# Optimization experiments

Measured on AMD Instinct MI355X. Metric: run time of the kernel, lower is better.

## Reference

```python
import jax, jax.numpy as jnp
import numpy as np

S, C1, C2, N = 4096, 2048, 2048, 1024


def setup_inputs() -> dict:
    key = jax.random.key(0)
    k1, k2, k3, k4 = jax.random.split(key, 4)
    # child log-likelihoods (samples, child_nodes); modest scale so exp() stays finite,
    # matching the (numerically naive) torch forward which exps without max-subtraction.
    ll1 = jax.random.normal(k1, (S, C1), dtype=jnp.float32)
    ll2 = jax.random.normal(k2, (S, C2), dtype=jnp.float32)
    # log edge weights, one tensor per child layer: (nodes, child_nodes)
    w1 = jax.random.normal(k3, (N, C1), dtype=jnp.float32)
    w2 = jax.random.normal(k4, (N, C2), dtype=jnp.float32)
    return {"ll1": ll1, "ll2": ll2, "w1": w1, "w2": w2}


def reference(ll1, ll2, w1, w2):
    # Per child layer: sum_c exp(ll[s,c] + w[n,c]) == exp(ll) @ exp(w).T  -> (S, N)
    # (same math as unsqueeze/repeat/exp/sum in the torch code, without the (S,C,N) blowup)
    result = jnp.exp(ll1) @ jnp.exp(w1).T + jnp.exp(ll2) @ jnp.exp(w2).T  # (S, N)
    # per-node log normalization constant over concatenated weights
    log_z = jax.nn.logsumexp(jnp.concatenate([w1, w2], axis=1), axis=1)  # (N,)
    return jnp.log(result) - log_z[None, :]
```

## Files before the change

kernel.cpp:

```cpp
#include <hip/hip_runtime.h>

#define S_DIM 4096
#define C_DIM 2048
#define N_DIM 1024
#define K_DIM 4096

#define BM2 256
#define BN2 256
#define KS 4
#define KSL (K_DIM / KS)
#define BK 32
#define NT2 (KSL / BK)
#define TILE2 32768
#define NBUF2 4

#define BM1 128
#define BN1 128
#define NT1 (K_DIM / BK)
#define TILE1 16384
#define NBUF1 8

typedef __attribute__((ext_vector_type(8))) short bf16x8;
typedef __attribute__((ext_vector_type(8))) unsigned short u16x8;
typedef __attribute__((ext_vector_type(4))) float f32x4;

__device__ static inline unsigned short f2bf(float f) {
    unsigned int u = __float_as_uint(f);
    u += 0x7FFFu + ((u >> 16) & 1u);
    return (unsigned short)(u >> 16);
}
__device__ static inline float bf2f(unsigned short h) {
    return __uint_as_float((unsigned int)h << 16);
}

__global__ void exp_ll_kernel(const float* __restrict__ ll1,
                              const float* __restrict__ ll2,
                              unsigned short* __restrict__ A) {
    const int total4 = S_DIM * C_DIM / 4;
    int stride = gridDim.x * blockDim.x;
    for (int i = blockIdx.x * blockDim.x + threadIdx.x; i < total4; i += stride) {
        int e = i << 2;
        int r = e >> 11;
        int c = e & 2047;
        size_t dst = ((size_t)r << 12) + c;
        float4 v = *reinterpret_cast<const float4*>(ll1 + e);
        ushort4 o;
        o.x = f2bf(__expf(v.x)); o.y = f2bf(__expf(v.y));
        o.z = f2bf(__expf(v.z)); o.w = f2bf(__expf(v.w));
        *reinterpret_cast<ushort4*>(A + dst) = o;
        float4 u = *reinterpret_cast<const float4*>(ll2 + e);
        ushort4 p;
        p.x = f2bf(__expf(u.x)); p.y = f2bf(__expf(u.y));
        p.z = f2bf(__expf(u.z)); p.w = f2bf(__expf(u.w));
        *reinterpret_cast<ushort4*>(A + dst + C_DIM) = p;
    }
}

__global__ void w_kernel(const float* __restrict__ w1,
                         const float* __restrict__ w2,
                         unsigned short* __restrict__ B,
                         float* __restrict__ lz) {
    const int n = blockIdx.x;
    const int tid = threadIdx.x;
    const int lane = tid & 63, wv = tid >> 6;
    const float* r1 = w1 + ((size_t)n << 11);
    const float* r2 = w2 + ((size_t)n << 11);
    float4 v0 = *reinterpret_cast<const float4*>(r1 + tid * 8);
    float4 v1 = *reinterpret_cast<const float4*>(r1 + tid * 8 + 4);
    float4 u0 = *reinterpret_cast<const float4*>(r2 + tid * 8);
    float4 u1 = *reinterpret_cast<const float4*>(r2 + tid * 8 + 4);

    float mx = fmaxf(fmaxf(fmaxf(v0.x, v0.y), fmaxf(v0.z, v0.w)),
                     fmaxf(fmaxf(v1.x, v1.y), fmaxf(v1.z, v1.w)));
    mx = fmaxf(mx, fmaxf(fmaxf(fmaxf(u0.x, u0.y), fmaxf(u0.z, u0.w)),
                          fmaxf(fmaxf(u1.x, u1.y), fmaxf(u1.z, u1.w))));
    #pragma unroll
    for (int off = 32; off > 0; off >>= 1) mx = fmaxf(mx, __shfl_xor(mx, off));
    __shared__ float red[4];
    if (lane == 0) red[wv] = mx;
    __syncthreads();
    mx = fmaxf(fmaxf(red[0], red[1]), fmaxf(red[2], red[3]));

    float s = __expf(v0.x - mx) + __expf(v0.y - mx) + __expf(v0.z - mx) + __expf(v0.w - mx)
            + __expf(v1.x - mx) + __expf(v1.y - mx) + __expf(v1.z - mx) + __expf(v1.w - mx)
            + __expf(u0.x - mx) + __expf(u0.y - mx) + __expf(u0.z - mx) + __expf(u0.w - mx)
            + __expf(u1.x - mx) + __expf(u1.y - mx) + __expf(u1.z - mx) + __expf(u1.w - mx);
    #pragma unroll
    for (int off = 32; off > 0; off >>= 1) s += __shfl_xor(s, off);
    __shared__ float red2[4];
    if (lane == 0) red2[wv] = s;
    __syncthreads();
    if (tid == 0)
        lz[n] = mx + __logf(red2[0] + red2[1] + red2[2] + red2[3]);

    unsigned short* brow = B + ((size_t)n << 12);
    ushort4 o;
    o.x = f2bf(__expf(v0.x)); o.y = f2bf(__expf(v0.y));
    o.z = f2bf(__expf(v0.z)); o.w = f2bf(__expf(v0.w));
    *reinterpret_cast<ushort4*>(brow + tid * 8) = o;
    o.x = f2bf(__expf(v1.x)); o.y = f2bf(__expf(v1.y));
    o.z = f2bf(__expf(v1.z)); o.w = f2bf(__expf(v1.w));
    *reinterpret_cast<ushort4*>(brow + tid * 8 + 4) = o;
    o.x = f2bf(__expf(u0.x)); o.y = f2bf(__expf(u0.y));
    o.z = f2bf(__expf(u0.z)); o.w = f2bf(__expf(u0.w));
    *reinterpret_cast<ushort4*>(brow + C_DIM + tid * 8) = o;
    o.x = f2bf(__expf(u1.x)); o.y = f2bf(__expf(u1.y));
    o.z = f2bf(__expf(u1.z)); o.w = f2bf(__expf(u1.w));
    *reinterpret_cast<ushort4*>(brow + C_DIM + tid * 8 + 4) = o;
}

typedef const unsigned int __attribute__((address_space(1)))* gas_ptr;
typedef unsigned int __attribute__((address_space(3)))* las_ptr;

__global__ __launch_bounds__(512, 1) void gemm_split_kernel(
        const unsigned short* __restrict__ A,
        const unsigned short* __restrict__ B,
        unsigned short* __restrict__ P) {
    __shared__ __align__(16) char lds[NBUF2 * TILE2];
    const int tid  = threadIdx.x;
    const int l    = tid & 63;
    const int w    = tid >> 6;
    const int wg   = blockIdx.x;
    const int x7   = wg & 7;
    const int bm   = (wg >> 3) & 15;
    const int c    = x7 + ((wg >> 7) << 3);
    const int ks   = c >> 2;
    const int bn   = c & 3;
    const int wr = w >> 1, wc = w & 1;
    const int lcol = l & 15, lk = l >> 4;

    const int kg = (l & 3) ^ ((l >> 3) & 3);
    const unsigned short* srcA0 = A + (size_t)(bm * BM2 + w * 16 + (l >> 2)) * K_DIM
                                    + ks * KSL + kg * 8;
    const unsigned short* srcA1 = srcA0 + (size_t)128 * K_DIM;
    const unsigned short* srcB0 = B + (size_t)(bn * BN2 + w * 16 + (l >> 2)) * K_DIM
                                    + ks * KSL + kg * 8;
    const unsigned short* srcB1 = srcB0 + (size_t)128 * K_DIM;
    const int dst0 = (w * 16 + (l >> 2)) * 64 + (l & 3) * 16;

    const int swz = (lk ^ ((lcol >> 1) & 3)) << 4;
    const int abase = (wr * 64 + lcol) * 64 + swz;
    const int bbase = 16384 + (wc * 128 + lcol) * 64 + swz;

    f32x4 acc[4][8] = {};
    bf16x8 a0[4], b0[8], a1[4], b1[8];

#define GLOAD(p_, o_) __builtin_amdgcn_global_load_lds((gas_ptr)(const void*)(p_), \
        (las_ptr)(void*)(lds + (o_)), 16, 0, 0)
#define STAGE2(T, BUFI) { const int _ko = (T) * BK; const int _bo = (BUFI) * TILE2;  \
        GLOAD(srcA0 + _ko, _bo + dst0);         GLOAD(srcA1 + _ko, _bo + dst0 + 8192); \
        GLOAD(srcB0 + _ko, _bo + dst0 + 16384); GLOAD(srcB1 + _ko, _bo + dst0 + 24576); }
#define READF2(RBUF, AR, BR) { const char* _rb = lds + (RBUF) * TILE2;               \
        _Pragma("unroll") for (int m = 0; m < 4; ++m)                                \
            AR[m] = *reinterpret_cast<const bf16x8*>(_rb + abase + m * 1024);        \
        _Pragma("unroll") for (int n = 0; n < 8; ++n)                                \
            BR[n] = *reinterpret_cast<const bf16x8*>(_rb + bbase + n * 1024); }
#define MFMAS2(AMM, BMM) {                                                           \
        __builtin_amdgcn_s_setprio(1);                                               \
        _Pragma("unroll") for (int m = 0; m < 4; ++m)                                \
            _Pragma("unroll") for (int n = 0; n < 8; ++n)                            \
                acc[m][n] = __builtin_amdgcn_mfma_f32_16x16x32_bf16(AMM[m], BMM[n],  \
                                                                    acc[m][n], 0, 0, 0); \
        __builtin_amdgcn_s_setprio(0); }
#define BODY2(RBUF, TS, SBUF, WAITN, DOSTAGE, AR, BR, AMM, BMM) {                    \
        asm volatile("s_waitcnt vmcnt(" #WAITN ")" ::: "memory");                    \
        __builtin_amdgcn_s_barrier();                                                \
        if (DOSTAGE) STAGE2(TS, SBUF);                                               \
        READF2(RBUF, AR, BR);                                                        \
        __builtin_amdgcn_sched_barrier(0);                                           \
        MFMAS2(AMM, BMM); }

    STAGE2(0, 0); STAGE2(1, 1); STAGE2(2, 2);
    asm volatile("s_waitcnt vmcnt(8)" ::: "memory");
    __builtin_amdgcn_s_barrier();
    READF2(0, a0, b0);
    for (int t4 = 0; t4 < NT2 - 4; t4 += 4) {
        BODY2(1, t4 + 3, 3, 4, 1, a1, b1, a0, b0);
        BODY2(2, t4 + 4, 0, 4, 1, a0, b0, a1, b1);
        BODY2(3, t4 + 5, 1, 4, 1, a1, b1, a0, b0);
        BODY2(0, t4 + 6, 2, 4, 1, a0, b0, a1, b1);
    }
    BODY2(1, 31, 3, 4, 1, a1, b1, a0, b0);
    BODY2(2, 0, 0, 4, 0, a0, b0, a1, b1);
    BODY2(3, 0, 0, 0, 0, a1, b1, a0, b0);
    MFMAS2(a1, b1);
#undef BODY2
#undef MFMAS2
#undef READF2
#undef STAGE2

    unsigned short* Pk = P + (size_t)ks * ((size_t)S_DIM * N_DIM);
    const int col_base = bn * BN2 + wc * 128;
    #pragma unroll
    for (int m = 0; m < 4; ++m) {
        const int row0 = bm * BM2 + wr * 64 + m * 16 + lk * 4;
        #pragma unroll
        for (int n = 0; n < 8; ++n) {
            const int col = col_base + n * 16 + lcol;
            #pragma unroll
            for (int j = 0; j < 4; ++j)
                Pk[(size_t)(row0 + j) * N_DIM + col] = f2bf(acc[m][n][j]);
        }
    }
#undef GLOAD
}

__global__ void reduce_kernel(const unsigned short* __restrict__ P,
                              const float* __restrict__ lz,
                              float* __restrict__ out) {
    const size_t SN = (size_t)S_DIM * N_DIM;
    int i = blockIdx.x * blockDim.x + threadIdx.x;
    size_t e = (size_t)i * 8;
    int n = (int)(e & (N_DIM - 1));
    u16x8 p0 = *reinterpret_cast<const u16x8*>(P + e);
    u16x8 p1 = *reinterpret_cast<const u16x8*>(P + SN + e);
    u16x8 p2 = *reinterpret_cast<const u16x8*>(P + 2 * SN + e);
    u16x8 p3 = *reinterpret_cast<const u16x8*>(P + 3 * SN + e);
    float4 lz0 = *reinterpret_cast<const float4*>(lz + n);
    float4 lz1 = *reinterpret_cast<const float4*>(lz + n + 4);
    float lzv[8] = {lz0.x, lz0.y, lz0.z, lz0.w, lz1.x, lz1.y, lz1.z, lz1.w};
    float o[8];
    #pragma unroll
    for (int j = 0; j < 8; ++j) {
        float s = bf2f((unsigned short)p0[j]) + bf2f((unsigned short)p1[j])
                + bf2f((unsigned short)p2[j]) + bf2f((unsigned short)p3[j]);
        o[j] = __logf(s) - lzv[j];
    }
    *reinterpret_cast<float4*>(out + e)     = make_float4(o[0], o[1], o[2], o[3]);
    *reinterpret_cast<float4*>(out + e + 4) = make_float4(o[4], o[5], o[6], o[7]);
}

__global__ __launch_bounds__(256, 1) void gemm_log_kernel128(
        const unsigned short* __restrict__ A,
        const unsigned short* __restrict__ B,
        const float* __restrict__ lz,
        float* __restrict__ out) {
    __shared__ __align__(16) char lds[NBUF1 * TILE1];
    const int tid  = threadIdx.x;
    const int l    = tid & 63;
    const int w    = tid >> 6;
    const int bn = blockIdx.x & 7;
    const int bm = blockIdx.x >> 3;
    const int wr = w >> 1, wc = w & 1;
    const int lcol = l & 15, lk = l >> 4;

    const int kg = (l & 3) ^ ((l >> 3) & 3);
    const unsigned short* src[4];
    int dst[4];
    #pragma unroll
    for (int i = 0; i < 4; ++i) {
        const int ri  = w * 4 + i;
        const int row = ri * 16 + (l >> 2);
        src[i] = (ri < 8)
            ? A + (size_t)(bm * BM1 + row) * K_DIM + kg * 8
            : B + (size_t)(bn * BN1 + row - 128) * K_DIM + kg * 8;
        dst[i] = row * 64 + (l & 3) * 16;
    }
    const int swz = (lk ^ ((lcol >> 1) & 3)) << 4;
    int aoff[4], boff[4];
    #pragma unroll
    for (int m = 0; m < 4; ++m) aoff[m] = (wr * 64 + m * 16 + lcol) * 64 + swz;
    #pragma unroll
    for (int n = 0; n < 4; ++n) boff[n] = 8192 + (wc * 64 + n * 16 + lcol) * 64 + swz;

    f32x4 acc[4][4] = {};
    bf16x8 a0[4], b0[4], a1[4], b1[4];

#define GLOAD(p_, o_) __builtin_amdgcn_global_load_lds((gas_ptr)(const void*)(p_), \
        (las_ptr)(void*)(lds + (o_)), 16, 0, 0)
#define STAGE(T, BUFI) { const int _ko = (T) * BK; const int _bo = (BUFI) * TILE1; \
        GLOAD(src[0] + _ko, _bo + dst[0]); GLOAD(src[1] + _ko, _bo + dst[1]);      \
        GLOAD(src[2] + _ko, _bo + dst[2]); GLOAD(src[3] + _ko, _bo + dst[3]); }
#define READF(RBUF, AR, BR) { const char* _rb = lds + (RBUF) * TILE1;              \
        _Pragma("unroll") for (int m = 0; m < 4; ++m)                              \
            AR[m] = *reinterpret_cast<const bf16x8*>(_rb + aoff[m]);               \
        _Pragma("unroll") for (int n = 0; n < 4; ++n)                              \
            BR[n] = *reinterpret_cast<const bf16x8*>(_rb + boff[n]); }
#define MFMAS(AMM, BMM)                                                            \
        _Pragma("unroll") for (int m = 0; m < 4; ++m)                              \
            _Pragma("unroll") for (int n = 0; n < 4; ++n)                          \
                acc[m][n] = __builtin_amdgcn_mfma_f32_16x16x32_bf16(AMM[m], BMM[n],\
                                                                    acc[m][n], 0, 0, 0);
#define BODY(T, SB, RB, WAITN, DOSTAGE, AR, BR, AMM, BMM) {                        \
        asm volatile("s_waitcnt vmcnt(" #WAITN ")" ::: "memory");                  \
        __builtin_amdgcn_s_barrier();                                              \
        if (DOSTAGE) STAGE((T) + 8, SB);                                           \
        READF(RB, AR, BR);                                                         \
        MFMAS(AMM, BMM); }

    STAGE(0, 0); STAGE(1, 1); STAGE(2, 2); STAGE(3, 3);
    STAGE(4, 4); STAGE(5, 5); STAGE(6, 6); STAGE(7, 7);
    asm volatile("s_waitcnt vmcnt(28)" ::: "memory");
    __builtin_amdgcn_s_barrier();
    READF(0, a0, b0);
    for (int t8 = 0; t8 < NT1 - 8; t8 += 8) {
        BODY(t8 + 0, 0, 1, 24, 1, a1, b1, a0, b0);
        BODY(t8 + 1, 1, 2, 24, 1, a0, b0, a1, b1);
        BODY(t8 + 2, 2, 3, 24, 1, a1, b1, a0, b0);
        BODY(t8 + 3, 3, 4, 24, 1, a0, b0, a1, b1);
        BODY(t8 + 4, 4, 5, 24, 1, a1, b1, a0, b0);
        BODY(t8 + 5, 5, 6, 24, 1, a0, b0, a1, b1);
        BODY(t8 + 6, 6, 7, 24, 1, a1, b1, a0, b0);
        BODY(t8 + 7, 7, 0, 24, 1, a0, b0, a1, b1);
    }
    BODY(120, 0, 1, 24, 0, a1, b1, a0, b0);
    BODY(121, 1, 2, 20, 0, a0, b0, a1, b1);
    BODY(122, 2, 3, 16, 0, a1, b1, a0, b0);
    BODY(123, 3, 4, 12, 0, a0, b0, a1, b1);
    BODY(124, 4, 5,  8, 0, a1, b1, a0, b0);
    BODY(125, 5, 6,  4, 0, a0, b0, a1, b1);
    BODY(126, 6, 7,  0, 0, a1, b1, a0, b0);
    MFMAS(a1, b1);
#undef BODY
#undef MFMAS
#undef READF
#undef STAGE
#undef GLOAD

    const int col_base = bn * BN1 + wc * 64;
    float lzv[4];
    #pragma unroll
    for (int n = 0; n < 4; ++n) lzv[n] = lz[col_base + n * 16 + lcol];
    #pragma unroll
    for (int m = 0; m < 4; ++m) {
        const int row0 = bm * BM1 + wr * 64 + m * 16 + lk * 4;
        #pragma unroll
        for (int n = 0; n < 4; ++n) {
            const int col = col_base + n * 16 + lcol;
            #pragma unroll
            for (int j = 0; j < 4; ++j)
                out[(size_t)(row0 + j) * N_DIM + col] = __logf(acc[m][n][j]) - lzv[n];
        }
    }
}

__global__ void naive_kernel(const float* __restrict__ ll1, const float* __restrict__ ll2,
                             const float* __restrict__ w1, const float* __restrict__ w2,
                             float* __restrict__ out) {
    int idx = blockIdx.x * blockDim.x + threadIdx.x;
    if (idx >= S_DIM * N_DIM) return;
    int s = idx >> 10, n = idx & (N_DIM - 1);
    const float* a1 = ll1 + (size_t)s * C_DIM;
    const float* a2 = ll2 + (size_t)s * C_DIM;
    const float* b1 = w1 + (size_t)n * C_DIM;
    const float* b2 = w2 + (size_t)n * C_DIM;
    float mx = -3.0e38f;
    for (int c = 0; c < C_DIM; ++c) mx = fmaxf(mx, b1[c]);
    for (int c = 0; c < C_DIM; ++c) mx = fmaxf(mx, b2[c]);
    float zs = 0.f, acc = 0.f;
    for (int c = 0; c < C_DIM; ++c) { zs += __expf(b1[c] - mx); acc += __expf(a1[c] + b1[c]); }
    for (int c = 0; c < C_DIM; ++c) { zs += __expf(b2[c] - mx); acc += __expf(a2[c] + b2[c]); }
    out[idx] = __logf(acc) - (mx + __logf(zs));
}

extern "C" void kernel_launch(void* const* d_in, const int* in_sizes, int n_in,
                              void* d_out, int out_size, void* d_ws, size_t ws_size,
                              hipStream_t stream) {
    const float* ll1 = (const float*)d_in[0];
    const float* ll2 = (const float*)d_in[1];
    const float* w1  = (const float*)d_in[2];
    const float* w2  = (const float*)d_in[3];
    float* out = (float*)d_out;

    const size_t a_elems = (size_t)S_DIM * K_DIM;
    const size_t b_elems = (size_t)N_DIM * K_DIM;
    const size_t sn      = (size_t)S_DIM * N_DIM;
    const size_t need1 = (a_elems + b_elems) * sizeof(unsigned short) + N_DIM * sizeof(float);
    const size_t need2 = need1 + KS * sn * sizeof(unsigned short);
    if (ws_size < need1) {
        naive_kernel<<<(S_DIM * N_DIM + 255) / 256, 256, 0, stream>>>(ll1, ll2, w1, w2, out);
        return;
    }
    unsigned short* Aws = (unsigned short*)d_ws;
    unsigned short* Bws = Aws + a_elems;
    float* lzws = (float*)(Bws + b_elems);

    exp_ll_kernel<<<2048, 256, 0, stream>>>(ll1, ll2, Aws);
    w_kernel<<<N_DIM, 256, 0, stream>>>(w1, w2, Bws, lzws);

    if (ws_size >= need2) {
        unsigned short* Pws = (unsigned short*)(lzws + N_DIM);
        gemm_split_kernel<<<(S_DIM / BM2) * (N_DIM / BN2) * KS, 512, 0, stream>>>(Aws, Bws, Pws);
        reduce_kernel<<<(int)(sn / 8 / 256), 256, 0, stream>>>(Pws, lzws, out);
    } else {
        gemm_log_kernel128<<<(S_DIM / BM1) * (N_DIM / BN1), 256, 0, stream>>>(Aws, Bws, lzws, out);
    }
}
```

Baseline: 78.91 us.

## Deepen GEMM LDS pipeline to five buffers and drop register double-buffering

The split-K GEMM kernel now keeps four tiles in flight using five LDS buffers instead of four, waiting on vmcnt(12) rather than vmcnt(4). The register ping-pong of A/B fragments, where the next tile's LDS reads overlapped the current tile's MFMAs under a sched_barrier, is replaced by a single fragment set read and consumed in the same step. The loop also uses runtime rotating buffer offsets instead of the manually unrolled four-way body. This hides more global load latency and frees registers, but exposes LDS read latency before the MFMAs, raises LDS use to 160KB which may limit occupancy, and adds per-iteration offset arithmetic.

```diff
diff --git a/kernel.cpp b/kernel.cpp
--- a/kernel.cpp
+++ b/kernel.cpp
@@ -12,7 +12,7 @@
 #define BK 32
 #define NT2 (KSL / BK)
 #define TILE2 32768
-#define NBUF2 4
+#define NBUF2 5
 
 #define BM1 128
 #define BN1 128
@@ -143,47 +143,44 @@
     const int bbase = 16384 + (wc * 128 + lcol) * 64 + swz;
 
     f32x4 acc[4][8] = {};
-    bf16x8 a0[4], b0[8], a1[4], b1[8];
+    bf16x8 a[4], b[8];
 
 #define GLOAD(p_, o_) __builtin_amdgcn_global_load_lds((gas_ptr)(const void*)(p_), \
         (las_ptr)(void*)(lds + (o_)), 16, 0, 0)
-#define STAGE2(T, BUFI) { const int _ko = (T) * BK; const int _bo = (BUFI) * TILE2;  \
+#define STAGE2(T, BO) { const int _ko = (T) * BK; const int _bo = (BO);              \
         GLOAD(srcA0 + _ko, _bo + dst0);         GLOAD(srcA1 + _ko, _bo + dst0 + 8192); \
         GLOAD(srcB0 + _ko, _bo + dst0 + 16384); GLOAD(srcB1 + _ko, _bo + dst0 + 24576); }
-#define READF2(RBUF, AR, BR) { const char* _rb = lds + (RBUF) * TILE2;               \
+#define READF2(BO) { const char* _rb = lds + (BO);                                   \
         _Pragma("unroll") for (int m = 0; m < 4; ++m)                                \
-            AR[m] = *reinterpret_cast<const bf16x8*>(_rb + abase + m * 1024);        \
+            a[m] = *reinterpret_cast<const bf16x8*>(_rb + abase + m * 1024);         \
         _Pragma("unroll") for (int n = 0; n < 8; ++n)                                \
-            BR[n] = *reinterpret_cast<const bf16x8*>(_rb + bbase + n * 1024); }
-#define MFMAS2(AMM, BMM) {                                                           \
+            b[n] = *reinterpret_cast<const bf16x8*>(_rb + bbase + n * 1024); }
+#define MFMAS2() {                                                                   \
         __builtin_amdgcn_s_setprio(1);                                               \
         _Pragma("unroll") for (int m = 0; m < 4; ++m)                                \
             _Pragma("unroll") for (int n = 0; n < 8; ++n)                            \
-                acc[m][n] = __builtin_amdgcn_mfma_f32_16x16x32_bf16(AMM[m], BMM[n],  \
+                acc[m][n] = __builtin_amdgcn_mfma_f32_16x16x32_bf16(a[m], b[n],      \
                                                                     acc[m][n], 0, 0, 0); \
         __builtin_amdgcn_s_setprio(0); }
-#define BODY2(RBUF, TS, SBUF, WAITN, DOSTAGE, AR, BR, AMM, BMM) {                    \
+#define BODY2(RBO, TS, SBO, WAITN, DOSTAGE) {                                        \
         asm volatile("s_waitcnt vmcnt(" #WAITN ")" ::: "memory");                    \
         __builtin_amdgcn_s_barrier();                                                \
-        if (DOSTAGE) STAGE2(TS, SBUF);                                               \
-        READF2(RBUF, AR, BR);                                                        \
-        __builtin_amdgcn_sched_barrier(0);                                           \
-        MFMAS2(AMM, BMM); }
-
-    STAGE2(0, 0); STAGE2(1, 1); STAGE2(2, 2);
-    asm volatile("s_waitcnt vmcnt(8)" ::: "memory");
-    __builtin_amdgcn_s_barrier();
-    READF2(0, a0, b0);
-    for (int t4 = 0; t4 < NT2 - 4; t4 += 4) {
-        BODY2(1, t4 + 3, 3, 4, 1, a1, b1, a0, b0);
-        BODY2(2, t4 + 4, 0, 4, 1, a0, b0, a1, b1);
-        BODY2(3, t4 + 5, 1, 4, 1, a1, b1, a0, b0);
-        BODY2(0, t4 + 6, 2, 4, 1, a0, b0, a1, b1);
-    }
-    BODY2(1, 31, 3, 4, 1, a1, b1, a0, b0);
-    BODY2(2, 0, 0, 4, 0, a0, b0, a1, b1);
-    BODY2(3, 0, 0, 0, 0, a1, b1, a0, b0);
-    MFMAS2(a1, b1);
+        if (DOSTAGE) STAGE2(TS, SBO);                                                \
+        READF2(RBO);                                                                 \
+        MFMAS2(); }
+
+    STAGE2(0, 0); STAGE2(1, TILE2); STAGE2(2, 2 * TILE2); STAGE2(3, 3 * TILE2);
+    int rbo = 0;
+    int sbo = 4 * TILE2;
+    for (int T = 0; T < NT2 - 4; ++T) {
+        BODY2(rbo, T + 4, sbo, 12, 1);
+        rbo += TILE2; if (rbo == NBUF2 * TILE2) rbo = 0;
+        sbo += TILE2; if (sbo == NBUF2 * TILE2) sbo = 0;
+    }
+    BODY2(rbo, 0, 0, 12, 0); rbo += TILE2; if (rbo == NBUF2 * TILE2) rbo = 0;
+    BODY2(rbo, 0, 0, 8, 0);  rbo += TILE2; if (rbo == NBUF2 * TILE2) rbo = 0;
+    BODY2(rbo, 0, 0, 4, 0);  rbo += TILE2; if (rbo == NBUF2 * TILE2) rbo = 0;
+    BODY2(rbo, 0, 0, 0, 0);
 #undef BODY2
 #undef MFMAS2
 #undef READF2
```

Result: faster. 73.85 us (-6.4%).
